# Performance work log

Hardware: AMD Instinct MI355X
Metric: run time of the kernel (lower is better)

## Reference

```python
import jax, jax.numpy as jnp
import numpy as np

IN_FEATURES = 1024
OUT_FEATURES = 1024
GRID_SIZE = 8
SPLINE_ORDER = 3
NUM_CTRL = GRID_SIZE + SPLINE_ORDER  # 11


def _make_grid():
    h = 2.0 / GRID_SIZE
    return jnp.linspace(-1.0 - SPLINE_ORDER * h, 1.0 + SPLINE_ORDER * h,
                        GRID_SIZE + 2 * SPLINE_ORDER + 1, dtype=jnp.float32)  # [15]


def b_splines(t, grid, order):
    # t: [B, F] (already tanh'd). Vectorized over all features at once —
    # the torch per-feature Python loop computes identical math per column.
    te = t[..., None]  # [B, F, 1]
    basis = ((te >= grid[:-1]) & (te < grid[1:])).astype(t.dtype)  # [B, F, G-1]
    for k in range(1, order + 1):
        left_den = grid[k:-1] - grid[:-k - 1]
        left_den = jnp.where(left_den == 0, jnp.ones_like(left_den), left_den)
        left = (te - grid[:-k - 1]) / left_den * basis[..., :-1]
        right_den = grid[k + 1:] - grid[1:-k]
        right_den = jnp.where(right_den == 0, jnp.ones_like(right_den), right_den)
        right = (grid[k + 1:] - te) / right_den * basis[..., 1:]
        basis = left + right
    return basis  # [B, F, NUM_CTRL]


def setup_inputs() -> dict:
    key = jax.random.key(0)
    kx, kc, kw = jax.random.split(key, 3)
    x = jax.random.normal(kx, (4096, IN_FEATURES), dtype=jnp.float32)
    coeffs = jax.random.normal(kc, (IN_FEATURES, OUT_FEATURES, NUM_CTRL), dtype=jnp.float32) * 0.05
    base_weight = jax.random.normal(kw, (IN_FEATURES, OUT_FEATURES), dtype=jnp.float32) * 0.05
    grid = _make_grid()
    return {"x": x, "coeffs": coeffs, "base_weight": base_weight, "grid": grid}


def reference(x, coeffs, base_weight, grid):
    bases = b_splines(jnp.tanh(x), grid, SPLINE_ORDER)          # [B, in, n]
    activation = jnp.einsum('bin,ion->bo', bases, coeffs)        # [B, out]
    residual = x @ base_weight                                   # [B, out]
    return activation + residual
```

## Files before the change

### kernel.cpp

```cpp
#include <hip/hip_runtime.h>
#include <hip/hip_bf16.h>

typedef __attribute__((ext_vector_type(8))) short bf16x8;
typedef __attribute__((ext_vector_type(4))) float f32x4;
typedef __attribute__((ext_vector_type(8))) unsigned short u16x8;

#define M_DIM 4096
#define N_DIM 1024
#define IN_F  1024
#define K_DIM 12288
#define KS2   2
#define KPART (K_DIM / KS2)
#define BK 64
#define NT (KPART / BK)

__device__ __forceinline__ unsigned short f2b(float v) {
  __hip_bfloat16 h = __float2bfloat16(v);
  return *reinterpret_cast<unsigned short*>(&h);
}

__device__ __forceinline__ void spline12(float xv, float* w) {
  float t  = tanhf(xv);
  float tf = (t + 1.75f) * 4.0f;
  int j = (int)tf;
  j = j < 3 ? 3 : (j > 10 ? 10 : j);
  float u  = tf - (float)j;
  float um = 1.0f - u;
  float u2 = u * u;
  float w0 = um * um * um * (1.0f / 6.0f);
  float w1 = (0.5f * u - 1.0f) * u2 + (2.0f / 3.0f);
  float w2 = ((-0.5f * u + 0.5f) * u + 0.5f) * u + (1.0f / 6.0f);
  float w3 = u * u2 * (1.0f / 6.0f);
  int base = j - 3;
  #pragma unroll
  for (int s = 0; s < 11; ++s) {
    int r = s - base;
    w[s] = (r == 0) ? w0 : (r == 1) ? w1 : (r == 2) ? w2 : (r == 3) ? w3 : 0.0f;
  }
  w[11] = xv;
}

__global__ __launch_bounds__(256) void bases_kernel(const float* __restrict__ x,
                                                    unsigned short* __restrict__ A) {
  __shared__ unsigned short sb[256 * 24];
  const int tid = threadIdx.x;
  int e0 = blockIdx.x * 512 + tid * 2;
  float2 xv = *(const float2*)(x + e0);
  float w0[12], w1[12];
  spline12(xv.x, w0);
  spline12(xv.y, w1);
  #pragma unroll
  for (int s = 0; s < 12; ++s) { sb[tid * 24 + s] = f2b(w0[s]); sb[tid * 24 + 12 + s] = f2b(w1[s]); }
  __syncthreads();
  u16x8* dst = (u16x8*)(A + (size_t)blockIdx.x * 512 * 12);
  const u16x8* src = (const u16x8*)sb;
  #pragma unroll
  for (int k = 0; k < 3; ++k) dst[tid + k * 256] = src[tid + k * 256];
}

__global__ __launch_bounds__(256) void repack_kernel(const float* __restrict__ coeffs,
                                                     const float* __restrict__ W,
                                                     unsigned short* __restrict__ Bt) {
  __shared__ float lc[64 * 180];
  __shared__ float lw[64 * 20];
  const int o0 = blockIdx.x * 16;
  const int i0 = blockIdx.y * 64;
  const int tid = threadIdx.x;
  #pragma unroll
  for (int it = 0; it < 11; ++it) {
    int v = it * 256 + tid;
    int i = v / 44, c = v - i * 44;
    f32x4 d = *(const f32x4*)(coeffs + ((size_t)(i0 + i) * 1024 + o0) * 11 + c * 4);
    *(f32x4*)(lc + i * 180 + c * 4) = d;
  }
  #pragma unroll
  for (int it = 0; it < 4; ++it) {
    int e = it * 256 + tid;
    int i = e >> 4, ol = e & 15;
    lw[i * 20 + ol] = W[(size_t)(i0 + i) * 1024 + o0 + ol];
  }
  __syncthreads();
  #pragma unroll
  for (int it = 0; it < 6; ++it) {
    int v = it * 256 + tid;
    int ol = v / 96, c = v - ol * 96;
    unsigned short h[8];
    #pragma unroll
    for (int s = 0; s < 8; ++s) {
      int g = c * 8 + s;
      int i = g / 12, n = g - i * 12;
      float val = (n < 11) ? lc[i * 180 + ol * 11 + n] : lw[i * 20 + ol];
      h[s] = f2b(val);
    }
    *(u16x8*)(Bt + (size_t)(o0 + ol) * K_DIM + (size_t)i0 * 12 + c * 8) =
        (u16x8){h[0], h[1], h[2], h[3], h[4], h[5], h[6], h[7]};
  }
}

__device__ __forceinline__ void async16(const void* g, void* l) {
  __builtin_amdgcn_global_load_lds(
      (const __attribute__((address_space(1))) void*)g,
      (__attribute__((address_space(3))) void*)l, 16, 0, 0);
}

__global__ __launch_bounds__(256, 2) void gemm_kernel(const unsigned short* __restrict__ A,
                                                      const unsigned short* __restrict__ Bt,
                                                      float* __restrict__ out) {
  __shared__ __align__(16) unsigned short lds[32768];
  char* lp = (char*)lds;
  const int AS[2] = {0, 16384};
  const int BS[2] = {32768, 49152};

  const int tid  = threadIdx.x;
  const int lane = tid & 63;
  const int wid  = tid >> 6;
  const int wm   = wid >> 1, wn = wid & 1;

  const int blk = blockIdx.x;
  const int xcd = blk & 7;
  const int idx = blk >> 3;
  const int bn  = idx & 7;
  const int p   = idx >> 3;
  const int bm  = xcd * 4 + (p & 3);
  const int ks  = p >> 2;
  const size_t m0 = (size_t)bm * 128;
  const size_t n0 = (size_t)bn * 128;
  const size_t ksbyte = (size_t)ks * KPART * 2;

  const char* srcA[4]; const char* srcB[4]; int ldso[4];
  #pragma unroll
  for (int q = 0; q < 4; ++q) {
    int g  = q * 256 + tid;
    int rr = g >> 3, cp = g & 7;
    int cs = cp ^ (rr & 7);
    srcA[q] = (const char*)A  + ((m0 + rr) * (size_t)K_DIM) * 2 + ksbyte + cs * 16;
    srcB[q] = (const char*)Bt + ((n0 + rr) * (size_t)K_DIM) * 2 + ksbyte + cs * 16;
    ldso[q] = g * 16;
  }

  auto stage = [&](int slot, int tile) {
    size_t kb = (size_t)tile * 128;
    #pragma unroll
    for (int q = 0; q < 4; ++q) async16(srcA[q] + kb, lp + AS[slot] + ldso[q]);
    #pragma unroll
    for (int q = 0; q < 4; ++q) async16(srcB[q] + kb, lp + BS[slot] + ldso[q]);
  };

  int offA[2][4], offB[2][4];
  #pragma unroll
  for (int kk = 0; kk < 2; ++kk) {
    #pragma unroll
    for (int m = 0; m < 4; ++m) {
      int row = wm * 64 + m * 16 + (lane & 15);
      int ck  = (kk * 4 + (lane >> 4)) ^ (row & 7);
      offA[kk][m] = row * 128 + ck * 16;
      int rowb = wn * 64 + m * 16 + (lane & 15);
      int ckb  = (kk * 4 + (lane >> 4)) ^ (rowb & 7);
      offB[kk][m] = rowb * 128 + ckb * 16;
    }
  }

  f32x4 acc[4][4];
  #pragma unroll
  for (int m = 0; m < 4; ++m)
    #pragma unroll
    for (int n = 0; n < 4; ++n) acc[m][n] = (f32x4){0.f, 0.f, 0.f, 0.f};

  stage(0, 0);
  stage(1, 1);

  for (int t = 0; t < NT; ++t) {
    const int cur = t & 1;
    if (t < NT - 1) asm volatile("s_waitcnt vmcnt(8)" ::: "memory");
    else            asm volatile("s_waitcnt vmcnt(0)" ::: "memory");
    __builtin_amdgcn_s_barrier();
    __builtin_amdgcn_sched_barrier(0);
    asm volatile("" ::: "memory");

    __builtin_amdgcn_s_setprio(1);
    #pragma unroll
    for (int kk = 0; kk < 2; ++kk) {
      bf16x8 a[4], b[4];
      #pragma unroll
      for (int m = 0; m < 4; ++m) a[m] = *(const bf16x8*)(lp + AS[cur] + offA[kk][m]);
      #pragma unroll
      for (int n = 0; n < 4; ++n) b[n] = *(const bf16x8*)(lp + BS[cur] + offB[kk][n]);
      #pragma unroll
      for (int m = 0; m < 4; ++m)
        #pragma unroll
        for (int n = 0; n < 4; ++n)
          acc[m][n] = __builtin_amdgcn_mfma_f32_16x16x32_bf16(a[m], b[n], acc[m][n], 0, 0, 0);
    }
    __builtin_amdgcn_s_setprio(0);

    asm volatile("" ::: "memory");
    __builtin_amdgcn_sched_barrier(0);
    __builtin_amdgcn_s_barrier();

    if (t + 2 < NT) stage(cur, t + 2);
  }

  const int lr = (lane >> 4) * 4;
  const int lc = lane & 15;
  #pragma unroll
  for (int m = 0; m < 4; ++m)
    #pragma unroll
    for (int n = 0; n < 4; ++n)
      #pragma unroll
      for (int j = 0; j < 4; ++j)
        atomicAdd(&out[(m0 + wm * 64 + m * 16 + lr + j) * N_DIM + n0 + wn * 64 + n * 16 + lc],
                  acc[m][n][j]);
}

__global__ __launch_bounds__(256) void fallback_kernel(const float* __restrict__ x,
                                                       const float* __restrict__ coeffs,
                                                       const float* __restrict__ W,
                                                       float* __restrict__ out) {
  __shared__ float bas[16][64][12];
  const int o0 = blockIdx.x * 64;
  const int b0 = blockIdx.y * 16;
  const int tid = threadIdx.x;
  const int o = tid & 63, bg = tid >> 6;
  float acc[4] = {0.f, 0.f, 0.f, 0.f};
  for (int ic = 0; ic < 16; ++ic) {
    __syncthreads();
    #pragma unroll
    for (int p = 0; p < 4; ++p) {
      int pp = tid + p * 256;
      int bb = pp >> 6, il = pp & 63;
      float w[12];
      spline12(x[(size_t)(b0 + bb) * 1024 + ic * 64 + il], w);
      #pragma unroll
      for (int n = 0; n < 12; ++n) bas[bb][il][n] = w[n];
    }
    __syncthreads();
    for (int il = 0; il < 64; ++il) {
      int gi = ic * 64 + il;
      const float* cp = coeffs + ((size_t)gi * 1024 + o0 + o) * 11;
      float cf[12];
      #pragma unroll
      for (int n = 0; n < 11; ++n) cf[n] = cp[n];
      cf[11] = W[(size_t)gi * 1024 + o0 + o];
      #pragma unroll
      for (int bb = 0; bb < 4; ++bb) {
        float s = 0.f;
        #pragma unroll
        for (int n = 0; n < 12; ++n) s += bas[bg * 4 + bb][il][n] * cf[n];
        acc[bb] += s;
      }
    }
  }
  #pragma unroll
  for (int bb = 0; bb < 4; ++bb)
    out[(size_t)(b0 + bg * 4 + bb) * 1024 + o0 + o] = acc[bb];
}

extern "C" void kernel_launch(void* const* d_in, const int* in_sizes, int n_in,
                              void* d_out, int out_size, void* d_ws, size_t ws_size,
                              hipStream_t stream) {
  const float* x      = (const float*)d_in[0];
  const float* coeffs = (const float*)d_in[1];
  const float* W      = (const float*)d_in[2];
  float* out = (float*)d_out;

  const size_t needA = (size_t)M_DIM * K_DIM * 2;
  const size_t needB = (size_t)N_DIM * K_DIM * 2;

  if (ws_size >= needA + needB) {
    unsigned short* Abuf = (unsigned short*)d_ws;
    unsigned short* Btuf = (unsigned short*)((char*)d_ws + needA);
    hipMemsetAsync(out, 0, (size_t)out_size * sizeof(float), stream);
    bases_kernel<<<dim3(M_DIM * IN_F / 512), dim3(256), 0, stream>>>(x, Abuf);
    repack_kernel<<<dim3(64, 16), dim3(256), 0, stream>>>(coeffs, W, Btuf);
    gemm_kernel<<<dim3(32 * 8 * KS2 / 2 * 2), dim3(256), 0, stream>>>(Abuf, Btuf, out);
  } else {
    fallback_kernel<<<dim3(16, 256), dim3(256), 0, stream>>>(x, coeffs, W, out);
  }
}
```

Baseline: 236.9 us.

## Enlarge GEMM tiles to 256x256 with 8 waves and 4-way split-K, use fast tanh

The bf16 MFMA GEMM tile grows from 128x128 with 4 waves to 256x256 with 8 waves. LDS doubles to 128KB and each wave now holds an 8x4 accumulator tile. Split-K goes from 2 to 4, so the grid stays at 256 blocks, about one per CU. The aim is to raise arithmetic intensity and reuse of the A/B tiles per global load, at the cost of doubling the fp32 atomic adds to the output and leaving room for only one block per CU. The spline basis kernel also swaps tanhf for an exp-based fast tanh to cut transcendental cost.

```diff
diff --git a/kernel.cpp b/kernel.cpp
--- a/kernel.cpp
+++ b/kernel.cpp
@@ -9,8 +9,8 @@
 #define N_DIM 1024
 #define IN_F  1024
 #define K_DIM 12288
-#define KS2   2
-#define KPART (K_DIM / KS2)
+#define KS4   4
+#define KPART (K_DIM / KS4)
 #define BK 64
 #define NT (KPART / BK)
 
@@ -19,8 +19,13 @@
   return *reinterpret_cast<unsigned short*>(&h);
 }
 
+__device__ __forceinline__ float fast_tanh(float x) {
+  float e = __expf(2.0f * x);
+  return 1.0f - 2.0f / (e + 1.0f);
+}
+
 __device__ __forceinline__ void spline12(float xv, float* w) {
-  float t  = tanhf(xv);
+  float t  = fast_tanh(xv);
   float tf = (t + 1.75f) * 4.0f;
   int j = (int)tf;
   j = j < 3 ? 3 : (j > 10 ? 10 : j);
@@ -103,66 +108,67 @@
       (__attribute__((address_space(3))) void*)l, 16, 0, 0);
 }
 
-__global__ __launch_bounds__(256, 2) void gemm_kernel(const unsigned short* __restrict__ A,
+__global__ __launch_bounds__(512, 2) void gemm_kernel(const unsigned short* __restrict__ A,
                                                       const unsigned short* __restrict__ Bt,
                                                       float* __restrict__ out) {
-  __shared__ __align__(16) unsigned short lds[32768];
+  __shared__ __align__(16) unsigned short lds[65536];
   char* lp = (char*)lds;
-  const int AS[2] = {0, 16384};
-  const int BS[2] = {32768, 49152};
+  const int AS[2] = {0, 32768};
+  const int BS[2] = {65536, 98304};
 
   const int tid  = threadIdx.x;
   const int lane = tid & 63;
   const int wid  = tid >> 6;
-  const int wm   = wid >> 1, wn = wid & 1;
+  const int wm   = wid >> 2;
+  const int wn   = wid & 3;
 
   const int blk = blockIdx.x;
   const int xcd = blk & 7;
-  const int idx = blk >> 3;
-  const int bn  = idx & 7;
-  const int p   = idx >> 3;
-  const int bm  = xcd * 4 + (p & 3);
-  const int ks  = p >> 2;
-  const size_t m0 = (size_t)bm * 128;
-  const size_t n0 = (size_t)bn * 128;
+  const int q   = blk >> 3;
+  const int bm  = xcd * 2 + (q & 1);
+  const int r2  = q >> 1;
+  const int bn  = r2 & 3;
+  const int ks  = r2 >> 2;
+  const size_t m0 = (size_t)bm * 256;
+  const size_t n0 = (size_t)bn * 256;
   const size_t ksbyte = (size_t)ks * KPART * 2;
 
   const char* srcA[4]; const char* srcB[4]; int ldso[4];
   #pragma unroll
-  for (int q = 0; q < 4; ++q) {
-    int g  = q * 256 + tid;
+  for (int p = 0; p < 4; ++p) {
+    int g  = p * 512 + tid;
     int rr = g >> 3, cp = g & 7;
     int cs = cp ^ (rr & 7);
-    srcA[q] = (const char*)A  + ((m0 + rr) * (size_t)K_DIM) * 2 + ksbyte + cs * 16;
-    srcB[q] = (const char*)Bt + ((n0 + rr) * (size_t)K_DIM) * 2 + ksbyte + cs * 16;
-    ldso[q] = g * 16;
+    srcA[p] = (const char*)A  + ((m0 + rr) * (size_t)K_DIM) * 2 + ksbyte + cs * 16;
+    srcB[p] = (const char*)Bt + ((n0 + rr) * (size_t)K_DIM) * 2 + ksbyte + cs * 16;
+    ldso[p] = g * 16;
   }
 
   auto stage = [&](int slot, int tile) {
     size_t kb = (size_t)tile * 128;
     #pragma unroll
-    for (int q = 0; q < 4; ++q) async16(srcA[q] + kb, lp + AS[slot] + ldso[q]);
-    #pragma unroll
-    for (int q = 0; q < 4; ++q) async16(srcB[q] + kb, lp + BS[slot] + ldso[q]);
+    for (int p = 0; p < 4; ++p) async16(srcA[p] + kb, lp + AS[slot] + ldso[p]);
+    #pragma unroll
+    for (int p = 0; p < 4; ++p) async16(srcB[p] + kb, lp + BS[slot] + ldso[p]);
   };
 
-  int offA[2][4], offB[2][4];
-  #pragma unroll
-  for (int kk = 0; kk < 2; ++kk) {
-    #pragma unroll
-    for (int m = 0; m < 4; ++m) {
-      int row = wm * 64 + m * 16 + (lane & 15);
-      int ck  = (kk * 4 + (lane >> 4)) ^ (row & 7);
-      offA[kk][m] = row * 128 + ck * 16;
-      int rowb = wn * 64 + m * 16 + (lane & 15);
-      int ckb  = (kk * 4 + (lane >> 4)) ^ (rowb & 7);
-      offB[kk][m] = rowb * 128 + ckb * 16;
-    }
-  }
-
-  f32x4 acc[4][4];
-  #pragma unroll
-  for (int m = 0; m < 4; ++m)
+  int offA[8], offB[4];
+  #pragma unroll
+  for (int m = 0; m < 8; ++m) {
+    int row = wm * 128 + m * 16 + (lane & 15);
+    int ck  = (lane >> 4) ^ (row & 7);
+    offA[m] = row * 128 + ck * 16;
+  }
+  #pragma unroll
+  for (int n = 0; n < 4; ++n) {
+    int rowb = wn * 64 + n * 16 + (lane & 15);
+    int ckb  = (lane >> 4) ^ (rowb & 7);
+    offB[n] = rowb * 128 + ckb * 16;
+  }
+
+  f32x4 acc[8][4];
+  #pragma unroll
+  for (int m = 0; m < 8; ++m)
     #pragma unroll
     for (int n = 0; n < 4; ++n) acc[m][n] = (f32x4){0.f, 0.f, 0.f, 0.f};
 
@@ -180,13 +186,14 @@
     __builtin_amdgcn_s_setprio(1);
     #pragma unroll
     for (int kk = 0; kk < 2; ++kk) {
-      bf16x8 a[4], b[4];
-      #pragma unroll
-      for (int m = 0; m < 4; ++m) a[m] = *(const bf16x8*)(lp + AS[cur] + offA[kk][m]);
-      #pragma unroll
-      for (int n = 0; n < 4; ++n) b[n] = *(const bf16x8*)(lp + BS[cur] + offB[kk][n]);
-      #pragma unroll
-      for (int m = 0; m < 4; ++m)
+      const int kx = kk * 64;
+      bf16x8 a[8], b[4];
+      #pragma unroll
+      for (int m = 0; m < 8; ++m) a[m] = *(const bf16x8*)(lp + AS[cur] + (offA[m] ^ kx));
+      #pragma unroll
+      for (int n = 0; n < 4; ++n) b[n] = *(const bf16x8*)(lp + BS[cur] + (offB[n] ^ kx));
+      #pragma unroll
+      for (int m = 0; m < 8; ++m)
         #pragma unroll
         for (int n = 0; n < 4; ++n)
           acc[m][n] = __builtin_amdgcn_mfma_f32_16x16x32_bf16(a[m], b[n], acc[m][n], 0, 0, 0);
@@ -203,12 +210,12 @@
   const int lr = (lane >> 4) * 4;
   const int lc = lane & 15;
   #pragma unroll
-  for (int m = 0; m < 4; ++m)
+  for (int m = 0; m < 8; ++m)
     #pragma unroll
     for (int n = 0; n < 4; ++n)
       #pragma unroll
       for (int j = 0; j < 4; ++j)
-        atomicAdd(&out[(m0 + wm * 64 + m * 16 + lr + j) * N_DIM + n0 + wn * 64 + n * 16 + lc],
+        atomicAdd(&out[(m0 + wm * 128 + m * 16 + lr + j) * N_DIM + n0 + wn * 64 + n * 16 + lc],
                   acc[m][n][j]);
 }
 
@@ -272,7 +279,7 @@
     hipMemsetAsync(out, 0, (size_t)out_size * sizeof(float), stream);
     bases_kernel<<<dim3(M_DIM * IN_F / 512), dim3(256), 0, stream>>>(x, Abuf);
     repack_kernel<<<dim3(64, 16), dim3(256), 0, stream>>>(coeffs, W, Btuf);
-    gemm_kernel<<<dim3(32 * 8 * KS2 / 2 * 2), dim3(256), 0, stream>>>(Abuf, Btuf, out);
+    gemm_kernel<<<dim3(256), dim3(512), 0, stream>>>(Abuf, Btuf, out);
   } else {
     fallback_kernel<<<dim3(16, 256), dim3(256), 0, stream>>>(x, coeffs, W, out);
   }
```

Result: slower. 263.8 us (+11.3%).
